# Kernel optimization log

Hardware: AMD Instinct MI355X
Metric: run time of the kernel (lower is better)

The kernel has to match this reference:

```python
import jax, jax.numpy as jnp
import numpy as np

NUM_HEADS = 12
DILATIONS = (1, 2, 4)
POOL_STRIDE = 2
LINFORMER_SEQ = 128


def setup_inputs() -> dict:
    key = jax.random.key(0)
    ks = jax.random.split(key, 8)
    B, N, C = 32, 1024, 768
    bank = 64
    return {
        "x": jax.random.normal(ks[0], (B, N, C), jnp.float32),
        "Wqkv": jax.random.normal(ks[1], (C, 3 * C), jnp.float32) * 0.02,
        "bqkv": jnp.zeros((3 * C,), jnp.float32),
        "E_k": jax.random.normal(ks[2], (LINFORMER_SEQ, 64), jnp.float32) * 0.02,
        "E_v": jax.random.normal(ks[3], (LINFORMER_SEQ, 64), jnp.float32) * 0.02,
        "Wproj": jax.random.normal(ks[4], (C, C), jnp.float32) * 0.02,
        "bproj": jnp.zeros((C,), jnp.float32),
        "k_bank": jax.random.normal(ks[5], (B, bank, C), jnp.float32),
        "v_bank": jax.random.normal(ks[6], (B, bank, C), jnp.float32),
    }


def reference(x, Wqkv, bqkv, E_k, E_v, Wproj, bproj, k_bank, v_bank):
    B, N, C = x.shape
    H = NUM_HEADS
    D = C // H
    S = int(np.sqrt(N))  # spatial side, N must be a perfect square

    # multi-scale dilated token gather
    xg = x.reshape(B, S, S, C)
    multi = [xg[:, ::d, ::d, :].reshape(B, -1, C) for d in DILATIONS]
    xm = jnp.concatenate(multi, axis=1)  # (B, NM, C)

    # landmark average pooling (kernel=stride=POOL_STRIDE, no padding)
    NM = xm.shape[1]
    NP = NM // POOL_STRIDE
    xp = xm[:, : NP * POOL_STRIDE].reshape(B, NP, POOL_STRIDE, C).mean(axis=2)

    # qkv on pooled landmarks, keep k and v heads
    qkv_p = (xp @ Wqkv + bqkv).reshape(B, NP, 3, H, D)
    k = qkv_p[:, :, 1].transpose(0, 2, 1, 3)  # (B,H,NP,D)
    v = qkv_p[:, :, 2].transpose(0, 2, 1, 3)

    # truncate/pad to Linformer seq_len (here NP=672 > 128 -> truncate)
    if k.shape[2] < LINFORMER_SEQ:
        pad = LINFORMER_SEQ - k.shape[2]
        k = jnp.pad(k, ((0, 0), (0, 0), (0, pad), (0, 0)))
        v = jnp.pad(v, ((0, 0), (0, 0), (0, pad), (0, 0)))
    else:
        k = k[:, :, :LINFORMER_SEQ]
        v = v[:, :, :LINFORMER_SEQ]

    # Linformer low-rank compression: E.T @ k
    kc = jnp.einsum('sc,bhsd->bhcd', E_k, k)  # (B,H,64,D)
    vc = jnp.einsum('sc,bhsd->bhcd', E_v, v)

    # memory bank heads
    kb = k_bank.reshape(B, -1, H, D).transpose(0, 2, 1, 3)
    vb = v_bank.reshape(B, -1, H, D).transpose(0, 2, 1, 3)
    k_full = jnp.concatenate([kc, kb], axis=2)  # (B,H,128,D)
    v_full = jnp.concatenate([vc, vb], axis=2)

    # queries from full-resolution tokens
    q = (x @ Wqkv + bqkv).reshape(B, N, 3, H, D)[:, :, 0].transpose(0, 2, 1, 3)

    # scaled dot-product attention (dropout p=0 in eval / reference)
    scale = 1.0 / jnp.sqrt(jnp.asarray(D, x.dtype))
    scores = jnp.einsum('bhqd,bhkd->bhqk', q, k_full) * scale
    attn = jax.nn.softmax(scores, axis=-1)
    out = jnp.einsum('bhqk,bhkd->bhqd', attn, v_full)

    out = out.transpose(0, 2, 1, 3).reshape(B, N, C)
    return out @ Wproj + bproj
```

## Files before the change

kernel.cpp:

```cpp
#include <hip/hip_runtime.h>

#define BB    32
#define NSEQ  1024
#define CDIM  768
#define NH    12
#define HD    64
#define LKEYS 128
#define NPOOL 128

typedef __bf16 bf16x8 __attribute__((ext_vector_type(8)));
typedef float  f32x4  __attribute__((ext_vector_type(4)));

__device__ __forceinline__ ushort f2bf(float f) {
    union { float f; uint u; } v; v.f = f;
    uint u = v.u;
    uint r = u + 0x7FFFu + ((u >> 16) & 1u);
    return (ushort)(r >> 16);
}
__device__ __forceinline__ uint pack2(float x, float y) {
    return (uint)f2bf(x) | ((uint)f2bf(y) << 16);
}

__global__ __launch_bounds__(256) void prep_kernel(
    const float* __restrict__ Wqkv, ushort* __restrict__ Wq_t,
    const float* __restrict__ Wproj, ushort* __restrict__ Wp_t,
    const float* __restrict__ x, ushort* __restrict__ xp)
{
    __shared__ ushort tile[32][33];
    int z = blockIdx.z;

    if (z == 2) {
        int flatb = blockIdx.y * 72 + blockIdx.x;
        if (flatb >= 1536) return;
        int idx = flatb * 256 + threadIdx.x;
        int c8 = idx % 96;
        int t  = idx / 96;
        int i  = t % NPOOL;
        int b  = t / NPOOL;
        if (b >= BB) return;
        const float4* x4 = (const float4*)x;
        size_t base0 = ((size_t)(b * NSEQ + 2 * i)) * 192 + c8 * 2;
        size_t base1 = base0 + 192;
        float4 a0 = x4[base0], a1 = x4[base0 + 1];
        float4 b0 = x4[base1], b1 = x4[base1 + 1];
        uint4 o;
        o.x = pack2(0.5f * (a0.x + b0.x), 0.5f * (a0.y + b0.y));
        o.y = pack2(0.5f * (a0.z + b0.z), 0.5f * (a0.w + b0.w));
        o.z = pack2(0.5f * (a1.x + b1.x), 0.5f * (a1.y + b1.y));
        o.w = pack2(0.5f * (a1.z + b1.z), 0.5f * (a1.w + b1.w));
        ((uint4*)xp)[idx] = o;
        return;
    }

    if (z == 1 && blockIdx.x >= 24) return;
    const float* src = z ? Wproj : Wqkv;
    ushort* dst      = z ? Wp_t  : Wq_t;
    int C = z ? CDIM : 3 * CDIM;
    const int R = CDIM;

    int bc = blockIdx.x * 32, br = blockIdx.y * 32;
    int tx = threadIdx.x & 31, ty = threadIdx.x >> 5;
#pragma unroll
    for (int i = 0; i < 32; i += 8)
        tile[ty + i][tx] = f2bf(src[(size_t)(br + ty + i) * C + bc + tx]);
    __syncthreads();
#pragma unroll
    for (int i = 0; i < 32; i += 8)
        dst[(size_t)(bc + ty + i) * R + br + tx] = tile[tx][ty + i];
}

__global__ __launch_bounds__(256) void cvt_bf16_kernel(const float* __restrict__ src,
                                                       ushort* __restrict__ dst, int n8)
{
    int idx = blockIdx.x * 256 + threadIdx.x;
    if (idx >= n8) return;
    float4 a = ((const float4*)src)[idx * 2];
    float4 b = ((const float4*)src)[idx * 2 + 1];
    uint4 o;
    o.x = pack2(a.x, a.y); o.y = pack2(a.z, a.w);
    o.z = pack2(b.x, b.y); o.w = pack2(b.z, b.w);
    ((uint4*)dst)[idx] = o;
}

template <bool OBF16>
__global__ __launch_bounds__(256) void mfma_gemm_kernel(
    const ushort* __restrict__ A, const ushort* __restrict__ Bt,
    const float* __restrict__ bias, void* __restrict__ Cout,
    int M, int N, int K)
{
    __shared__ ushort As[128 * 32];
    __shared__ ushort Bs[128 * 32];

    int tid  = threadIdx.x;
    int wave = tid >> 6, lane = tid & 63;

    int nwg  = gridDim.x * gridDim.y;
    int bid  = blockIdx.y * gridDim.x + blockIdx.x;
    int q    = nwg >> 3, r = nwg & 7;
    int xcd  = bid & 7, j = bid >> 3;
    int flat = (xcd < r ? xcd * (q + 1) : r * (q + 1) + (xcd - r) * q) + j;
    int n0 = (flat % gridDim.x) * 128;
    int m0 = (flat / gridDim.x) * 128;

    int wm = wave >> 1, wn = wave & 1;
    int lm = lane & 15, lh = lane >> 4;

    f32x4 acc[4][4] = {};

    for (int k0 = 0; k0 < K; k0 += 32) {
        __syncthreads();
#pragma unroll
        for (int t = 0; t < 2; t++) {
            int fl = wave * 128 + t * 64 + lane;
            int row = fl >> 2, kc = (fl & 3) * 8;
            const ushort* gA = A  + (size_t)(m0 + row) * K + k0 + kc;
            const ushort* gB = Bt + (size_t)(n0 + row) * K + k0 + kc;
            __builtin_amdgcn_global_load_lds(
                (const __attribute__((address_space(1))) void*)gA,
                (__attribute__((address_space(3))) void*)(As + (size_t)(wave * 128 + t * 64) * 8),
                16, 0, 0);
            __builtin_amdgcn_global_load_lds(
                (const __attribute__((address_space(1))) void*)gB,
                (__attribute__((address_space(3))) void*)(Bs + (size_t)(wave * 128 + t * 64) * 8),
                16, 0, 0);
        }
        __syncthreads();

        bf16x8 af[4], bfr[4];
#pragma unroll
        for (int i = 0; i < 4; i++)
            af[i] = *(const bf16x8*)((const void*)&As[(wm * 64 + i * 16 + lm) * 32 + lh * 8]);
#pragma unroll
        for (int jj = 0; jj < 4; jj++)
            bfr[jj] = *(const bf16x8*)((const void*)&Bs[(wn * 64 + jj * 16 + lm) * 32 + lh * 8]);
#pragma unroll
        for (int i = 0; i < 4; i++)
#pragma unroll
            for (int jj = 0; jj < 4; jj++)
                acc[i][jj] = __builtin_amdgcn_mfma_f32_16x16x32_bf16(af[i], bfr[jj], acc[i][jj], 0, 0, 0);
    }

    int crow = m0 + wm * 64, ccol = n0 + wn * 64;
#pragma unroll
    for (int jj = 0; jj < 4; jj++) {
        int col = ccol + jj * 16 + lm;
        float bb = bias[col];
        if constexpr (OBF16) {
            ushort* C = (ushort*)Cout;
#pragma unroll
            for (int i = 0; i < 4; i++)
#pragma unroll
                for (int rr = 0; rr < 4; rr++)
                    C[(size_t)(crow + i * 16 + lh * 4 + rr) * N + col] = f2bf(acc[i][jj][rr] + bb);
        } else {
            float* C = (float*)Cout;
#pragma unroll
            for (int i = 0; i < 4; i++)
#pragma unroll
                for (int rr = 0; rr < 4; rr++)
                    C[(size_t)(crow + i * 16 + lh * 4 + rr) * N + col] = acc[i][jj][rr] + bb;
        }
    }
}

template <bool OBF16>
__global__ __launch_bounds__(256) void gemm_db_kernel(
    const ushort* __restrict__ A, const ushort* __restrict__ Bt,
    const float* __restrict__ bias, void* __restrict__ Cout,
    int M, int N, int K)
{
    __shared__ ushort As[2][128 * 64];
    __shared__ ushort Bs[2][128 * 64];

    int tid  = threadIdx.x;
    int lane = tid & 63;
    int wave = tid >> 6;

    int nwg  = gridDim.x * gridDim.y;
    int bid  = blockIdx.y * gridDim.x + blockIdx.x;
    int q    = nwg >> 3, r = nwg & 7;
    int xcd  = bid & 7, jj0 = bid >> 3;
    int flat = (xcd < r ? xcd * (q + 1) : r * (q + 1) + (xcd - r) * q) + jj0;
    int n0 = (flat % gridDim.x) * 128;
    int m0 = (flat / gridDim.x) * 128;

    int wm = wave >> 1, wn = wave & 1;
    int lm = lane & 15, lh = lane >> 4;

    const int NT = K >> 6;

    auto stageB = [&](int tt) {
        int slot = tt & 1;
#pragma unroll
        for (int ld = 0; ld < 4; ld++) {
            int c = ld * 256 + tid;
            int prow = c >> 3, pch = c & 7;
            int lch = pch ^ (prow & 7);
            const ushort* g = Bt + (size_t)(n0 + prow) * K + tt * 64 + lch * 8;
            __builtin_amdgcn_global_load_lds(
                (const __attribute__((address_space(1))) void*)g,
                (__attribute__((address_space(3))) void*)(&Bs[slot][c * 8]),
                16, 0, 0);
        }
    };
    auto stageA16 = [&](int tt) {
        int slot = tt & 1;
#pragma unroll
        for (int ld = 0; ld < 4; ld++) {
            int c = ld * 256 + tid;
            int prow = c >> 3, pch = c & 7;
            int lch = pch ^ (prow & 7);
            const ushort* g = A + (size_t)(m0 + prow) * K + tt * 64 + lch * 8;
            __builtin_amdgcn_global_load_lds(
                (const __attribute__((address_space(1))) void*)g,
                (__attribute__((address_space(3))) void*)(&As[slot][c * 8]),
                16, 0, 0);
        }
    };

    f32x4 acc[4][4] = {};

    auto compute = [&](int slot) {
        bf16x8 bfr[4], af[4];
#pragma unroll
        for (int ks = 0; ks < 2; ks++) {
#pragma unroll
            for (int jj = 0; jj < 4; jj++) {
                int rn = wn * 64 + jj * 16 + lm;
                int ch = (ks * 4 + lh) ^ (rn & 7);
                bfr[jj] = *(const bf16x8*)((const void*)&Bs[slot][rn * 64 + ch * 8]);
            }
#pragma unroll
            for (int i = 0; i < 4; i++) {
                int rm = wm * 64 + i * 16 + lm;
                int ch = (ks * 4 + lh) ^ (rm & 7);
                af[i] = *(const bf16x8*)((const void*)&As[slot][rm * 64 + ch * 8]);
            }
            __builtin_amdgcn_s_setprio(1);
#pragma unroll
            for (int i = 0; i < 4; i++)
#pragma unroll
                for (int jj = 0; jj < 4; jj++)
                    acc[i][jj] = __builtin_amdgcn_mfma_f32_16x16x32_bf16(af[i], bfr[jj], acc[i][jj], 0, 0, 0);
            __builtin_amdgcn_s_setprio(0);
        }
    };

    stageA16(0); stageB(0);
    stageA16(1); stageB(1);
    for (int t = 0; t < NT; t++) {
        int slot = t & 1;
        if (t + 1 < NT) asm volatile("s_waitcnt vmcnt(8)" ::: "memory");
        else            asm volatile("s_waitcnt vmcnt(0)" ::: "memory");
        __builtin_amdgcn_s_barrier();
        asm volatile("" ::: "memory");
        compute(slot);
        __builtin_amdgcn_s_barrier();
        asm volatile("" ::: "memory");
        if (t + 2 < NT) { stageA16(t + 2); stageB(t + 2); }
    }

    int crow = m0 + wm * 64, ccol = n0 + wn * 64;
#pragma unroll
    for (int jj = 0; jj < 4; jj++) {
        int col = ccol + jj * 16 + lm;
        float bb = bias[col];
        if constexpr (OBF16) {
            ushort* C = (ushort*)Cout;
#pragma unroll
            for (int i = 0; i < 4; i++)
#pragma unroll
                for (int rr = 0; rr < 4; rr++)
                    C[(size_t)(crow + i * 16 + lh * 4 + rr) * N + col] = f2bf(acc[i][jj][rr] + bb);
        } else {
            float* C = (float*)Cout;
#pragma unroll
            for (int i = 0; i < 4; i++)
#pragma unroll
                for (int rr = 0; rr < 4; rr++)
                    C[(size_t)(crow + i * 16 + lh * 4 + rr) * N + col] = acc[i][jj][rr] + bb;
        }
    }
}

__global__ __launch_bounds__(256) void compress_kernel(
    const float* __restrict__ kvp,
    const float* __restrict__ Ek, const float* __restrict__ Ev,
    const float* __restrict__ kbank, const float* __restrict__ vbank,
    ushort* __restrict__ kfull, ushort* __restrict__ vfullT)
{
    __shared__ float Es[128 * 64];
    __shared__ float Sl[128 * 64];

    int tid = threadIdx.x;
    int h = blockIdx.x, b = blockIdx.y, which = blockIdx.z;
    const float* E    = which ? Ev : Ek;
    const float* bank = which ? vbank : kbank;

#pragma unroll
    for (int i = 0; i < 8; i++) {
        int flat = tid + i * 256;
        *(float4*)&Es[flat * 4] = *(const float4*)&E[flat * 4];
    }
    const float* src = kvp + (size_t)b * 128 * 1536 + which * 768 + h * HD;
#pragma unroll
    for (int i = 0; i < 8; i++) {
        int flat = tid + i * 256;
        int s = flat >> 4, d4 = flat & 15;
        *(float4*)&Sl[s * 64 + d4 * 4] = *(const float4*)&src[(size_t)s * 1536 + d4 * 4];
    }

    const float* bankbase = bank + (size_t)b * 64 * CDIM + h * HD;
    ushort* outK = kfull  + (size_t)(b * NH + h) * LKEYS * HD;
    ushort* outV = vfullT + (size_t)(b * NH + h) * HD * LKEYS;

#pragma unroll
    for (int i = 0; i < 4; i++) {
        int flat = tid + i * 256;
        int j = flat >> 4, d4 = flat & 15;
        float4 v = *(const float4*)&bankbase[(size_t)j * CDIM + d4 * 4];
        if (!which) {
            ushort4 o;
            o.x = f2bf(v.x); o.y = f2bf(v.y); o.z = f2bf(v.z); o.w = f2bf(v.w);
            *(ushort4*)&outK[(size_t)(64 + j) * HD + d4 * 4] = o;
        } else {
            outV[(size_t)(d4 * 4 + 0) * LKEYS + 64 + j] = f2bf(v.x);
            outV[(size_t)(d4 * 4 + 1) * LKEYS + 64 + j] = f2bf(v.y);
            outV[(size_t)(d4 * 4 + 2) * LKEYS + 64 + j] = f2bf(v.z);
            outV[(size_t)(d4 * 4 + 3) * LKEYS + 64 + j] = f2bf(v.w);
        }
    }
    __syncthreads();

    int tx = tid & 15, ty = tid >> 4;
    float acc[4][4];
#pragma unroll
    for (int i = 0; i < 4; i++)
#pragma unroll
        for (int j = 0; j < 4; j++) acc[i][j] = 0.f;

#pragma unroll 4
    for (int s = 0; s < 128; s++) {
        float4 av = *(const float4*)&Es[s * 64 + ty * 4];
        float4 bv = *(const float4*)&Sl[s * 64 + tx * 4];
        float a[4] = {av.x, av.y, av.z, av.w};
        float bb[4] = {bv.x, bv.y, bv.z, bv.w};
#pragma unroll
        for (int i = 0; i < 4; i++)
#pragma unroll
            for (int j = 0; j < 4; j++)
                acc[i][j] += a[i] * bb[j];
    }
    if (!which) {
#pragma unroll
        for (int i = 0; i < 4; i++) {
            ushort4 o;
            o.x = f2bf(acc[i][0]); o.y = f2bf(acc[i][1]);
            o.z = f2bf(acc[i][2]); o.w = f2bf(acc[i][3]);
            *(ushort4*)&outK[(size_t)(ty * 4 + i) * HD + tx * 4] = o;
        }
    } else {
#pragma unroll
        for (int i = 0; i < 4; i++)
#pragma unroll
            for (int j = 0; j < 4; j++)
                outV[(size_t)(tx * 4 + j) * LKEYS + ty * 4 + i] = f2bf(acc[i][j]);
    }
}

__global__ __launch_bounds__(256) void attn_mfma_kernel(
    const ushort* __restrict__ qb, const ushort* __restrict__ kf,
    const ushort* __restrict__ vt, ushort* __restrict__ ob)
{
    __shared__ __align__(16) ushort lds[64 * 72 + 128 * 72 + 64 * 136];
    ushort* Qs = lds;
    ushort* Ks = lds + 64 * 72;
    ushort* Vs = lds + 64 * 72 + 128 * 72;
    ushort* Ps = lds;

    int tid  = threadIdx.x;
    int wave = tid >> 6, lane = tid & 63;
    int lm = lane & 15, lh = lane >> 4;
    int qt = blockIdx.x, h = blockIdx.y, b = blockIdx.z;

    const ushort* qbase = qb + ((size_t)(b * NSEQ + qt * 64)) * CDIM + h * HD;
    const ushort* kbase = kf + (size_t)(b * NH + h) * LKEYS * HD;
    const ushort* vbase = vt + (size_t)(b * NH + h) * HD * LKEYS;

#pragma unroll
    for (int it = 0; it < 2; it++) {
        int flat = tid + it * 256;
        int row = flat >> 3, seg = flat & 7;
        *(uint4*)&Qs[row * 72 + seg * 8] = *(const uint4*)&qbase[(size_t)row * CDIM + seg * 8];
    }
#pragma unroll
    for (int it = 0; it < 4; it++) {
        int flat = tid + it * 256;
        int row = flat >> 3, seg = flat & 7;
        *(uint4*)&Ks[row * 72 + seg * 8] = *(const uint4*)&kbase[(size_t)row * HD + seg * 8];
    }
#pragma unroll
    for (int it = 0; it < 4; it++) {
        int flat = tid + it * 256;
        int row = flat >> 4, seg = flat & 15;
        *(uint4*)&Vs[row * 136 + seg * 8] = *(const uint4*)&vbase[(size_t)row * LKEYS + seg * 8];
    }
    __syncthreads();

    f32x4 sacc[8] = {};
    bf16x8 aq[2];
#pragma unroll
    for (int ks = 0; ks < 2; ks++)
        aq[ks] = *(const bf16x8*)((const void*)&Qs[(wave * 16 + lm) * 72 + ks * 32 + lh * 8]);
#pragma unroll
    for (int j = 0; j < 8; j++)
#pragma unroll
        for (int ks = 0; ks < 2; ks++) {
            bf16x8 bk = *(const bf16x8*)((const void*)&Ks[(j * 16 + lm) * 72 + ks * 32 + lh * 8]);
            sacc[j] = __builtin_amdgcn_mfma_f32_16x16x32_bf16(aq[ks], bk, sacc[j], 0, 0, 0);
        }

    float rinv[4];
#pragma unroll
    for (int r = 0; r < 4; r++) {
        float m = sacc[0][r];
#pragma unroll
        for (int j = 1; j < 8; j++) m = fmaxf(m, sacc[j][r]);
#pragma unroll
        for (int off = 1; off < 16; off <<= 1) m = fmaxf(m, __shfl_xor(m, off, 64));
        float s = 0.f;
#pragma unroll
        for (int j = 0; j < 8; j++) {
            float e = __expf((sacc[j][r] - m) * 0.125f);
            sacc[j][r] = e;
            s += e;
        }
#pragma unroll
        for (int off = 1; off < 16; off <<= 1) s += __shfl_xor(s, off, 64);
        rinv[r] = 1.f / s;
    }

    __syncthreads();
#pragma unroll
    for (int j = 0; j < 8; j++)
#pragma unroll
        for (int r = 0; r < 4; r++)
            Ps[(size_t)(wave * 16 + lh * 4 + r) * 136 + j * 16 + lm] = f2bf(sacc[j][r] * rinv[r]);
    __syncthreads();

    f32x4 oacc[4] = {};
#pragma unroll
    for (int ks = 0; ks < 4; ks++) {
        bf16x8 ap = *(const bf16x8*)((const void*)&Ps[(wave * 16 + lm) * 136 + ks * 32 + lh * 8]);
#pragma unroll
        for (int j = 0; j < 4; j++) {
            bf16x8 bv = *(const bf16x8*)((const void*)&Vs[(j * 16 + lm) * 136 + ks * 32 + lh * 8]);
            oacc[j] = __builtin_amdgcn_mfma_f32_16x16x32_bf16(ap, bv, oacc[j], 0, 0, 0);
        }
    }

    ushort* obase = ob + ((size_t)(b * NSEQ + qt * 64)) * CDIM + h * HD;
#pragma unroll
    for (int j = 0; j < 4; j++)
#pragma unroll
        for (int r = 0; r < 4; r++)
            obase[(size_t)(wave * 16 + lh * 4 + r) * CDIM + j * 16 + lm] = f2bf(oacc[j][r]);
}

extern "C" void kernel_launch(void* const* d_in, const int* in_sizes, int n_in,
                              void* d_out, int out_size, void* d_ws, size_t ws_size,
                              hipStream_t stream)
{
    const float* x     = (const float*)d_in[0];
    const float* Wqkv  = (const float*)d_in[1];
    const float* bqkv  = (const float*)d_in[2];
    const float* Ek    = (const float*)d_in[3];
    const float* Ev    = (const float*)d_in[4];
    const float* Wproj = (const float*)d_in[5];
    const float* bproj = (const float*)d_in[6];
    const float* kbank = (const float*)d_in[7];
    const float* vbank = (const float*)d_in[8];
    float* out = (float*)d_out;
    float* ws  = (float*)d_ws;

    float*  kvp    = ws;
    ushort* qb_bf  = (ushort*)ws;
    ushort* x_bf   = (ushort*)(ws + 12582912);
    ushort* aob    = x_bf;
    ushort* xp_bf  = (ushort*)(ws + 25165824);
    ushort* Wq_t   = (ushort*)(ws + 26738688);
    ushort* Wp_t   = (ushort*)(ws + 27623424);
    ushort* k_full = (ushort*)(ws + 27918336);
    ushort* v_fullT= (ushort*)(ws + 29491200);

    prep_kernel<<<dim3(72, 24, 3), 256, 0, stream>>>(Wqkv, Wq_t, Wproj, Wp_t, x, xp_bf);
    cvt_bf16_kernel<<<12288, 256, 0, stream>>>(x, x_bf, 3145728);

    mfma_gemm_kernel<false><<<dim3(12, 32), 256, 0, stream>>>(
        xp_bf, Wq_t + (size_t)CDIM * CDIM, bqkv + CDIM, kvp, 4096, 2 * CDIM, CDIM);
    compress_kernel<<<dim3(NH, BB, 2), 256, 0, stream>>>(
        kvp, Ek, Ev, kbank, vbank, k_full, v_fullT);

    gemm_db_kernel<true><<<dim3(6, 256), 256, 0, stream>>>(
        x_bf, Wq_t, bqkv, qb_bf, BB * NSEQ, CDIM, CDIM);

    attn_mfma_kernel<<<dim3(16, NH, BB), 256, 0, stream>>>(qb_bf, k_full, v_fullT, aob);

    gemm_db_kernel<false><<<dim3(6, 256), 256, 0, stream>>>(
        aob, Wp_t, bproj, out, BB * NSEQ, CDIM, CDIM);
}
```

Before: 374.5 us.

## Fuse x bf16 conversion into Q GEMM and merge with KV GEMM launch

Removes the separate fp32-to-bf16 conversion pass over x by having the Q projection GEMM load fp32 x tiles into LDS and convert them on the fly with v_cvt_pk_bf16_f32. The Q GEMM and the pooled KV GEMM become one launch that dispatches on block index, with XOR-swizzled LDS layouts. This drops one full read/write of x in bf16 and two kernel launches. In exchange the Q GEMM loses the double-buffered gemm_db pipeline, uses a single-buffered 32-wide K loop, and reads twice as many bytes of A from global.

```diff
diff --git a/kernel.cpp b/kernel.cpp
--- a/kernel.cpp
+++ b/kernel.cpp
@@ -19,6 +19,11 @@
 }
 __device__ __forceinline__ uint pack2(float x, float y) {
     return (uint)f2bf(x) | ((uint)f2bf(y) << 16);
+}
+__device__ __forceinline__ uint cvtpk(float lo, float hi) {
+    uint u;
+    asm("v_cvt_pk_bf16_f32 %0, %1, %2" : "=v"(u) : "v"(lo), "v"(hi));
+    return u;
 }
 
 __global__ __launch_bounds__(256) void prep_kernel(
@@ -69,96 +74,145 @@
         dst[(size_t)(bc + ty + i) * R + br + tx] = tile[tx][ty + i];
 }
 
-__global__ __launch_bounds__(256) void cvt_bf16_kernel(const float* __restrict__ src,
-                                                       ushort* __restrict__ dst, int n8)
+__global__ __launch_bounds__(256) void qkv_kernel(
+    const float* __restrict__ x, const ushort* __restrict__ xp,
+    const ushort* __restrict__ Wq_t, const float* __restrict__ bqkv,
+    ushort* __restrict__ qb, float* __restrict__ kvp)
 {
-    int idx = blockIdx.x * 256 + threadIdx.x;
-    if (idx >= n8) return;
-    float4 a = ((const float4*)src)[idx * 2];
-    float4 b = ((const float4*)src)[idx * 2 + 1];
-    uint4 o;
-    o.x = pack2(a.x, a.y); o.y = pack2(a.z, a.w);
-    o.z = pack2(b.x, b.y); o.w = pack2(b.z, b.w);
-    ((uint4*)dst)[idx] = o;
-}
-
-template <bool OBF16>
-__global__ __launch_bounds__(256) void mfma_gemm_kernel(
-    const ushort* __restrict__ A, const ushort* __restrict__ Bt,
-    const float* __restrict__ bias, void* __restrict__ Cout,
-    int M, int N, int K)
-{
-    __shared__ ushort As[128 * 32];
-    __shared__ ushort Bs[128 * 32];
-
-    int tid  = threadIdx.x;
-    int wave = tid >> 6, lane = tid & 63;
-
-    int nwg  = gridDim.x * gridDim.y;
-    int bid  = blockIdx.y * gridDim.x + blockIdx.x;
-    int q    = nwg >> 3, r = nwg & 7;
-    int xcd  = bid & 7, j = bid >> 3;
-    int flat = (xcd < r ? xcd * (q + 1) : r * (q + 1) + (xcd - r) * q) + j;
-    int n0 = (flat % gridDim.x) * 128;
-    int m0 = (flat / gridDim.x) * 128;
-
+    __shared__ __align__(16) unsigned char smem[24 * 1024];
+
+    int tid = threadIdx.x, wave = tid >> 6, lane = tid & 63;
     int wm = wave >> 1, wn = wave & 1;
     int lm = lane & 15, lh = lane >> 4;
 
+    int bid0 = blockIdx.x;
+    int cpx  = gridDim.x >> 3;
+    int bid  = (bid0 & 7) * cpx + (bid0 >> 3);
+
     f32x4 acc[4][4] = {};
 
-    for (int k0 = 0; k0 < K; k0 += 32) {
-        __syncthreads();
-#pragma unroll
-        for (int t = 0; t < 2; t++) {
-            int fl = wave * 128 + t * 64 + lane;
-            int row = fl >> 2, kc = (fl & 3) * 8;
-            const ushort* gA = A  + (size_t)(m0 + row) * K + k0 + kc;
-            const ushort* gB = Bt + (size_t)(n0 + row) * K + k0 + kc;
-            __builtin_amdgcn_global_load_lds(
-                (const __attribute__((address_space(1))) void*)gA,
-                (__attribute__((address_space(3))) void*)(As + (size_t)(wave * 128 + t * 64) * 8),
-                16, 0, 0);
-            __builtin_amdgcn_global_load_lds(
-                (const __attribute__((address_space(1))) void*)gB,
-                (__attribute__((address_space(3))) void*)(Bs + (size_t)(wave * 128 + t * 64) * 8),
-                16, 0, 0);
-        }
-        __syncthreads();
-
-        bf16x8 af[4], bfr[4];
-#pragma unroll
-        for (int i = 0; i < 4; i++)
-            af[i] = *(const bf16x8*)((const void*)&As[(wm * 64 + i * 16 + lm) * 32 + lh * 8]);
-#pragma unroll
-        for (int jj = 0; jj < 4; jj++)
-            bfr[jj] = *(const bf16x8*)((const void*)&Bs[(wn * 64 + jj * 16 + lm) * 32 + lh * 8]);
-#pragma unroll
-        for (int i = 0; i < 4; i++)
-#pragma unroll
-            for (int jj = 0; jj < 4; jj++)
-                acc[i][jj] = __builtin_amdgcn_mfma_f32_16x16x32_bf16(af[i], bfr[jj], acc[i][jj], 0, 0, 0);
-    }
-
-    int crow = m0 + wm * 64, ccol = n0 + wn * 64;
-#pragma unroll
-    for (int jj = 0; jj < 4; jj++) {
-        int col = ccol + jj * 16 + lm;
-        float bb = bias[col];
-        if constexpr (OBF16) {
-            ushort* C = (ushort*)Cout;
+    if (bid < 1536) {
+        float*  As = (float*)smem;
+        ushort* Bs = (ushort*)(smem + 16384);
+        int n0 = (bid % 6) * 128, m0 = (bid / 6) * 128;
+
+        for (int k0 = 0; k0 < CDIM; k0 += 32) {
+            __syncthreads();
+#pragma unroll
+            for (int ld = 0; ld < 4; ld++) {
+                int fl = ld * 256 + tid;
+                int row = fl >> 3, pch = fl & 7;
+                int lch = pch ^ (row & 7);
+                const float* g = x + (size_t)(m0 + row) * CDIM + k0 + lch * 4;
+                __builtin_amdgcn_global_load_lds(
+                    (const __attribute__((address_space(1))) void*)g,
+                    (__attribute__((address_space(3))) void*)(As + fl * 4),
+                    16, 0, 0);
+            }
+#pragma unroll
+            for (int ld = 0; ld < 2; ld++) {
+                int fl = ld * 256 + tid;
+                int row = fl >> 2, pch = fl & 3;
+                int lch = pch ^ (row & 3);
+                const ushort* g = Wq_t + (size_t)(n0 + row) * CDIM + k0 + lch * 8;
+                __builtin_amdgcn_global_load_lds(
+                    (const __attribute__((address_space(1))) void*)g,
+                    (__attribute__((address_space(3))) void*)(Bs + fl * 8),
+                    16, 0, 0);
+            }
+            __syncthreads();
+
+            bf16x8 af[4], bfr[4];
+#pragma unroll
+            for (int jj = 0; jj < 4; jj++) {
+                int rn = wn * 64 + jj * 16 + lm;
+                bfr[jj] = *(const bf16x8*)((const void*)&Bs[rn * 32 + ((lh ^ (rn & 3)) * 8)]);
+            }
+#pragma unroll
+            for (int i = 0; i < 4; i++) {
+                int rm = wm * 64 + i * 16 + lm;
+                int s = rm & 7;
+                float4 fa = *(const float4*)&As[rm * 32 + (((2 * lh)     ^ s) * 4)];
+                float4 fb = *(const float4*)&As[rm * 32 + (((2 * lh + 1) ^ s) * 4)];
+                uint4 u;
+                u.x = cvtpk(fa.x, fa.y); u.y = cvtpk(fa.z, fa.w);
+                u.z = cvtpk(fb.x, fb.y); u.w = cvtpk(fb.z, fb.w);
+                af[i] = *(const bf16x8*)((const void*)&u);
+            }
+#pragma unroll
+            for (int i = 0; i < 4; i++)
+#pragma unroll
+                for (int jj = 0; jj < 4; jj++)
+                    acc[i][jj] = __builtin_amdgcn_mfma_f32_16x16x32_bf16(af[i], bfr[jj], acc[i][jj], 0, 0, 0);
+        }
+
+        int crow = m0 + wm * 64, ccol = n0 + wn * 64;
+#pragma unroll
+        for (int jj = 0; jj < 4; jj++) {
+            int col = ccol + jj * 16 + lm;
+            float bb = bqkv[col];
 #pragma unroll
             for (int i = 0; i < 4; i++)
 #pragma unroll
                 for (int rr = 0; rr < 4; rr++)
-                    C[(size_t)(crow + i * 16 + lh * 4 + rr) * N + col] = f2bf(acc[i][jj][rr] + bb);
-        } else {
-            float* C = (float*)Cout;
+                    qb[(size_t)(crow + i * 16 + lh * 4 + rr) * CDIM + col] = f2bf(acc[i][jj][rr] + bb);
+        }
+    } else {
+        ushort* As = (ushort*)smem;
+        ushort* Bs = (ushort*)(smem + 8192);
+        int b2 = bid - 1536;
+        int n0 = (b2 % 12) * 128, m0 = (b2 / 12) * 128;
+        const ushort* Bt = Wq_t + (size_t)CDIM * CDIM;
+        const int NKV = 2 * CDIM;
+
+        for (int k0 = 0; k0 < CDIM; k0 += 32) {
+            __syncthreads();
+#pragma unroll
+            for (int ld = 0; ld < 2; ld++) {
+                int fl = ld * 256 + tid;
+                int row = fl >> 2, pch = fl & 3;
+                int lch = pch ^ (row & 3);
+                const ushort* gA = xp + (size_t)(m0 + row) * CDIM + k0 + lch * 8;
+                const ushort* gB = Bt + (size_t)(n0 + row) * CDIM + k0 + lch * 8;
+                __builtin_amdgcn_global_load_lds(
+                    (const __attribute__((address_space(1))) void*)gA,
+                    (__attribute__((address_space(3))) void*)(As + fl * 8),
+                    16, 0, 0);
+                __builtin_amdgcn_global_load_lds(
+                    (const __attribute__((address_space(1))) void*)gB,
+                    (__attribute__((address_space(3))) void*)(Bs + fl * 8),
+                    16, 0, 0);
+            }
+            __syncthreads();
+
+            bf16x8 af[4], bfr[4];
+#pragma unroll
+            for (int jj = 0; jj < 4; jj++) {
+                int rn = wn * 64 + jj * 16 + lm;
+                bfr[jj] = *(const bf16x8*)((const void*)&Bs[rn * 32 + ((lh ^ (rn & 3)) * 8)]);
+            }
+#pragma unroll
+            for (int i = 0; i < 4; i++) {
+                int rm = wm * 64 + i * 16 + lm;
+                af[i] = *(const bf16x8*)((const void*)&As[rm * 32 + ((lh ^ (rm & 3)) * 8)]);
+            }
+#pragma unroll
+            for (int i = 0; i < 4; i++)
+#pragma unroll
+                for (int jj = 0; jj < 4; jj++)
+                    acc[i][jj] = __builtin_amdgcn_mfma_f32_16x16x32_bf16(af[i], bfr[jj], acc[i][jj], 0, 0, 0);
+        }
+
+        int crow = m0 + wm * 64, ccol = n0 + wn * 64;
+#pragma unroll
+        for (int jj = 0; jj < 4; jj++) {
+            int col = ccol + jj * 16 + lm;
+            float bb = bqkv[CDIM + col];
 #pragma unroll
             for (int i = 0; i < 4; i++)
 #pragma unroll
                 for (int rr = 0; rr < 4; rr++)
-                    C[(size_t)(crow + i * 16 + lh * 4 + rr) * N + col] = acc[i][jj][rr] + bb;
+                    kvp[(size_t)(crow + i * 16 + lh * 4 + rr) * NKV + col] = acc[i][jj][rr] + bb;
         }
     }
 }
@@ -484,26 +538,21 @@
     float* ws  = (float*)d_ws;
 
     float*  kvp    = ws;
-    ushort* qb_bf  = (ushort*)ws;
-    ushort* x_bf   = (ushort*)(ws + 12582912);
-    ushort* aob    = x_bf;
-    ushort* xp_bf  = (ushort*)(ws + 25165824);
-    ushort* Wq_t   = (ushort*)(ws + 26738688);
-    ushort* Wp_t   = (ushort*)(ws + 27623424);
-    ushort* k_full = (ushort*)(ws + 27918336);
-    ushort* v_fullT= (ushort*)(ws + 29491200);
+    ushort* qb_bf  = (ushort*)(ws + 6291456);
+    ushort* aob    = (ushort*)(ws + 18874368);
+    ushort* xp_bf  = (ushort*)(ws + 31457280);
+    ushort* Wq_t   = (ushort*)(ws + 33030144);
+    ushort* Wp_t   = (ushort*)(ws + 33914880);
+    ushort* k_full = (ushort*)(ws + 34209792);
+    ushort* v_fullT= (ushort*)(ws + 35782656);
 
     prep_kernel<<<dim3(72, 24, 3), 256, 0, stream>>>(Wqkv, Wq_t, Wproj, Wp_t, x, xp_bf);
-    cvt_bf16_kernel<<<12288, 256, 0, stream>>>(x, x_bf, 3145728);
-
-    mfma_gemm_kernel<false><<<dim3(12, 32), 256, 0, stream>>>(
-        xp_bf, Wq_t + (size_t)CDIM * CDIM, bqkv + CDIM, kvp, 4096, 2 * CDIM, CDIM);
+
+    qkv_kernel<<<1920, 256, 0, stream>>>(x, xp_bf, Wq_t, bqkv, qb_bf, kvp);
+
     compress_kernel<<<dim3(NH, BB, 2), 256, 0, stream>>>(
         kvp, Ek, Ev, kbank, vbank, k_full, v_fullT);
 
-    gemm_db_kernel<true><<<dim3(6, 256), 256, 0, stream>>>(
-        x_bf, Wq_t, bqkv, qb_bf, BB * NSEQ, CDIM, CDIM);
-
     attn_mfma_kernel<<<dim3(16, NH, BB), 256, 0, stream>>>(qb_bf, k_full, v_fullT, aob);
 
     gemm_db_kernel<false><<<dim3(6, 256), 256, 0, stream>>>(
```

Measured after the change: 417.9 us. +11.6%, slower.
